# Kernel optimization log

Measured on AMD Instinct MI355X. Metric: run time of the kernel, lower is better.

## Reference

```python
import jax, jax.numpy as jnp
import numpy as np

RADII = [2, 4]
EPS = 1e-6


def _avg_pool_hw(t, k):
    # valid avg-pool with kernel k, stride 1 over the last two dims
    nd = t.ndim
    win = (1,) * (nd - 2) + (k, k)
    s = jax.lax.reduce_window(t, 0.0, jax.lax.add, win, (1,) * nd, 'VALID')
    return s / float(k * k)


def _patch_cca(x, y, r):
    B, C1, H, W = x.shape
    C2 = y.shape[1]
    k = 2 * r + 1
    pad = ((0, 0), (0, 0), (r, r), (r, r))
    xp = jnp.pad(x, pad, mode='reflect')  # (B,C1,Hp,Wp)
    yp = jnp.pad(y, pad, mode='reflect')  # (B,C2,Hp,Wp)

    # local second moments via outer products + avg pooling
    xx = _avg_pool_hw(xp[:, :, None] * xp[:, None], k)  # (B,C1,C1,H,W)
    yy = _avg_pool_hw(yp[:, :, None] * yp[:, None], k)  # (B,C2,C2,H,W)
    xy = _avg_pool_hw(xp[:, :, None] * yp[:, None], k)  # (B,C1,C2,H,W)
    xm = _avg_pool_hw(xp, k)  # (B,C1,H,W)
    ym = _avg_pool_hw(yp, k)  # (B,C2,H,W)

    cxx = xx - xm[:, :, None] * xm[:, None]
    cyy = yy - ym[:, :, None] * ym[:, None]
    cxy = xy - xm[:, :, None] * ym[:, None]

    # move matrix dims last: (B,H,W,Ci,Cj)
    cxx = jnp.transpose(cxx, (0, 3, 4, 1, 2)) + EPS * jnp.eye(C1, dtype=x.dtype)
    cyy = jnp.transpose(cyy, (0, 3, 4, 1, 2)) + EPS * jnp.eye(C2, dtype=x.dtype)
    cxy = jnp.transpose(cxy, (0, 3, 4, 1, 2))

    lx_inv = jnp.linalg.inv(jnp.linalg.cholesky(cxx))  # (B,H,W,C1,C1)
    ly_inv = jnp.linalg.inv(jnp.linalg.cholesky(cyy))  # (B,H,W,C2,C2)
    corr = jnp.einsum('bhwij,bhwjk,bhwkl->bhwil', lx_inv, cxy, ly_inv)
    diag = jnp.diagonal(corr, axis1=-2, axis2=-1)  # (B,H,W,min(C1,C2))
    sim = jnp.abs(diag).sum(-1) / min(C1, C2)  # (B,H,W)
    return sim[:, None]  # (B,1,H,W)


def setup_inputs() -> dict:
    key = jax.random.key(0)
    kx, ky = jax.random.split(key)
    B, C, H, W = 2, 6, 512, 512
    x = jax.random.normal(kx, (B, C, H, W), dtype=jnp.float32)
    y = jax.random.normal(ky, (B, C, H, W), dtype=jnp.float32)
    return {'x': x, 'y': y}


def reference(x, y):
    # stack per-radius CCA maps on a trailing axis -> (B,1,H,W,len(RADII))
    return jnp.stack([_patch_cca(x, y, r) for r in RADII], axis=-1)
```

## Files before the change

### kernel.cpp

```cpp
#include <hip/hip_runtime.h>
#include <math.h>

typedef float v2f __attribute__((ext_vector_type(2)));
typedef float v4f __attribute__((ext_vector_type(4)));

#define LT(i,j) ((i)*((i)+1)/2 + (j))

__device__ __forceinline__ int reflect512(int i) {
  int a = (i < 0) ? -i : i;
  int b = 1022 - a;
  return (a < b) ? a : b;
}

constexpr int HB   = 520;
constexpr int RSP  = HB * 4;
constexpr int PSTR = 2 * HB * HB * 4;

__global__ __launch_bounds__(256)
void prep_planar_t(const float* __restrict__ xg, const float* __restrict__ yg,
                   float* __restrict__ zb) {
  constexpr int H = 512, W = 512, HW = H * W;
  constexpr int WQ  = HB / 4;
  constexpr int PER = 2 * HB * WQ;
  const int idx = blockIdx.x * 256 + threadIdx.x;
  if (idx >= 3 * PER) return;
  const int p  = idx / PER;
  int r        = idx - p * PER;
  const int b  = r / (HB * WQ);
  r           -= b * (HB * WQ);
  const int hr = r / WQ;
  const int q  = r - hr * WQ;
  const int h  = reflect512(hr - 4);
  const int w0 = q * 4 - 4;

  float v[4][4];
  #pragma unroll
  for (int c = 0; c < 4; ++c) {
    const int ch = 4 * p + c;
    const float* src = (ch < 6 ? xg : yg)
                     + (size_t)b * 6 * HW + (size_t)(ch % 6) * HW
                     + (size_t)h * W;
    if (w0 >= 0 && w0 + 3 < W) {
      const v4f t = *(const v4f*)(src + w0);
      #pragma unroll
      for (int j = 0; j < 4; ++j) v[c][j] = t[j];
    } else {
      #pragma unroll
      for (int j = 0; j < 4; ++j) v[c][j] = src[reflect512(w0 + j)];
    }
  }

  float* o = zb + (size_t)p * PSTR + ((size_t)(b * HB + hr) * HB + q * 4) * 4;
  #pragma unroll
  for (int j = 0; j < 4; ++j) {
    v4f t = {v[0][j], v[1][j], v[2][j], v[3][j]};
    *(v4f*)(o + j * 4) = t;
  }
}

__device__ __forceinline__ float gget(const v2f* accd, const v2f* accs,
                                      int a, int b) {
  const int t = LT(a >> 1, b >> 1);
  if (((a & 1) == 0) && ((b & 1) == 0)) return accd[t].x;
  if (((a & 1) == 1) && ((b & 1) == 1)) return accd[t].y;
  if ((a & 1) == 0) return accs[t].x;
  return accs[t].y;
}

__device__ __forceinline__ void cholinv6(float* a) {
  #pragma unroll
  for (int j = 0; j < 6; ++j) {
    float d = a[LT(j,j)];
    #pragma unroll
    for (int p = 0; p < j; ++p) d -= a[LT(j,p)] * a[LT(j,p)];
    const float rd = __builtin_amdgcn_rsqf(d);
    a[LT(j,j)] = rd;
    #pragma unroll
    for (int i = j + 1; i < 6; ++i) {
      float s = a[LT(i,j)];
      #pragma unroll
      for (int p = 0; p < j; ++p) s -= a[LT(i,p)] * a[LT(j,p)];
      a[LT(i,j)] = s * rd;
    }
  }
  #pragma unroll
  for (int j = 0; j < 6; ++j) {
    #pragma unroll
    for (int i = j + 1; i < 6; ++i) {
      float s = 0.0f;
      #pragma unroll
      for (int p = j; p < i; ++p) s += a[LT(i,p)] * a[LT(p,j)];
      a[LT(i,j)] = -s * a[LT(i,i)];
    }
  }
}

template <bool ADD>
__device__ __forceinline__ void px_acc(const float* __restrict__ p,
                                       v2f* zs, v2f* accd, v2f* accs) {
  const v4f l0 = *(const v4f*)(p + 0 * PSTR);
  const v4f l1 = *(const v4f*)(p + 1 * PSTR);
  const v4f l2 = *(const v4f*)(p + 2 * PSTR);
  v2f z[6];
  z[0] = l0.lo; z[1] = l0.hi;
  z[2] = l1.lo; z[3] = l1.hi;
  z[4] = l2.lo; z[5] = l2.hi;
  #pragma unroll
  for (int q = 0; q < 6; ++q) zs[q] = ADD ? (zs[q] + z[q]) : (zs[q] - z[q]);
  int t = 0;
  #pragma unroll
  for (int Kp = 0; Kp < 6; ++Kp) {
    #pragma unroll
    for (int Pp = 0; Pp <= Kp; ++Pp) {
      const v2f c  = z[Pp];
      const v2f cs = __builtin_shufflevector(c, c, 1, 0);
      const v2f a  = ADD ? z[Kp] : -z[Kp];
      accd[t] = __builtin_elementwise_fma(a, c,  accd[t]);
      accs[t] = __builtin_elementwise_fma(a, cs, accs[t]);
      ++t;
    }
  }
}

template <int K, bool ADD>
__device__ __forceinline__ void row_acc_g(const float* __restrict__ p,
                                          v2f* zs, v2f* accd, v2f* accs) {
  #pragma unroll
  for (int dx = 0; dx < K; ++dx) px_acc<ADD>(p + dx * 4, zs, accd, accs);
}

template <int K>
__device__ __forceinline__ void extract_emit(const v2f* zs, const v2f* accd,
                                             const v2f* accs,
                                             float* ax, float* ay, float* cxy) {
  constexpr float inv_n = 1.0f / (K * K);
  float mx[6], my[6];
  #pragma unroll
  for (int i = 0; i < 6; ++i) {
    mx[i] = ((i & 1) ? zs[i >> 1].y : zs[i >> 1].x) * inv_n;
    my[i] = ((i & 1) ? zs[3 + (i >> 1)].y : zs[3 + (i >> 1)].x) * inv_n;
  }
  {
    int t = 0;
    #pragma unroll
    for (int i = 0; i < 6; ++i)
      #pragma unroll
      for (int j = 0; j <= i; ++j) {
        const float e = (i == j) ? 1e-6f : 0.0f;
        ax[t] = gget(accd, accs, i, j) * inv_n - mx[i] * mx[j] + e;
        ay[t] = gget(accd, accs, 6 + i, 6 + j) * inv_n - my[i] * my[j] + e;
        ++t;
      }
  }
  #pragma unroll
  for (int i = 0; i < 6; ++i)
    #pragma unroll
    for (int j = 0; j < 6; ++j)
      cxy[i * 6 + j] = fmaf(-mx[i], my[j], gget(accd, accs, 6 + j, i) * inv_n);
}

__device__ __forceinline__ float finish_sim(float* ax, float* ay,
                                            const float* cxy) {
  cholinv6(ax);
  cholinv6(ay);
  float sim = 0.0f;
  #pragma unroll
  for (int i = 0; i < 6; ++i) {
    float di = 0.0f;
    #pragma unroll
    for (int j = 0; j <= i; ++j) {
      float inner = 0.0f;
      #pragma unroll
      for (int k = i; k < 6; ++k) inner += cxy[j * 6 + k] * ay[LT(k, i)];
      di += ax[LT(i, j)] * inner;
    }
    sim += fabsf(di);
  }
  return sim * (1.0f / 6.0f);
}

template <int R, int V>
__device__ __forceinline__ void run(const float* __restrict__ zb,
                                    float* __restrict__ out, int b, int ri) {
  constexpr int K = 2 * R + 1;
  constexpr int H = 512, W = 512;

  const int h0 = blockIdx.y * (16 * V);
  const int w0 = blockIdx.x * 16;
  const int tx = threadIdx.x & 15;
  const int g  = threadIdx.x >> 4;
  const int hbase = h0 + g * V;
  const int wc = w0 + tx;

  const float* base = zb +
      ((size_t)(b * HB + (hbase + 4 - R)) * HB + (wc + 4 - R)) * 4;

  v2f zs[6]    = {};
  v2f accd[21] = {};
  v2f accs[21] = {};

  #pragma unroll 1
  for (int dy = 0; dy < K; ++dy)
    row_acc_g<K, true>(base + dy * RSP, zs, accd, accs);

  float ax[21], ay[21], cxy[36];
  extract_emit<K>(zs, accd, accs, ax, ay, cxy);

  #pragma unroll 1
  for (int s = 1; s < V; ++s) {
    row_acc_g<K, true >(base + (s + 2 * R) * RSP, zs, accd, accs);
    row_acc_g<K, false>(base + (s - 1)     * RSP, zs, accd, accs);
    out[((size_t)((b * H + hbase + s - 1) * W + wc)) * 2 + ri] =
        finish_sim(ax, ay, cxy);
    extract_emit<K>(zs, accd, accs, ax, ay, cxy);
  }
  out[((size_t)((b * H + hbase + V - 1) * W + wc)) * 2 + ri] =
      finish_sim(ax, ay, cxy);
}

__global__ __launch_bounds__(256, 2)
void cca_planar(const float* __restrict__ zb, float* __restrict__ out) {
  const int z = blockIdx.z;
  if (z < 2) run<2, 8>(zb, out, z, 0);
  else       run<4, 8>(zb, out, z - 2, 1);
}

extern "C" void kernel_launch(void* const* d_in, const int* in_sizes, int n_in,
                              void* d_out, int out_size, void* d_ws, size_t ws_size,
                              hipStream_t stream) {
  const float* x = (const float*)d_in[0];
  const float* y = (const float*)d_in[1];
  float* out = (float*)d_out;
  float* zb  = (float*)d_ws;

  {
    const int n = 3 * 2 * HB * (HB / 4);
    prep_planar_t<<<dim3((n + 255) / 256), dim3(256), 0, stream>>>(x, y, zb);
  }
  dim3 grid(512 / 16, 512 / (16 * 8), 4);
  cca_planar<<<grid, dim3(256), 0, stream>>>(zb, out);
}
```

Baseline: 137.4 us.

## Fuse prep and CCA kernels with a software grid barrier

Merges the planar-transpose prep kernel into the main CCA kernel. Each of the 512 blocks first does a grid-strided share of the prep work, then all blocks wait on a global atomic counter barrier before computing. This removes one kernel launch and the gap between the two kernels. In exchange it relies on all 512 blocks being co-resident, which launch_bounds(256,2) on a 256-CU part should allow. The generation counter makes the barrier reusable across calls, but it adds spin-wait and fence costs.

```diff
diff --git a/kernel.cpp b/kernel.cpp
--- a/kernel.cpp
+++ b/kernel.cpp
@@ -16,14 +16,15 @@
 constexpr int RSP  = HB * 4;
 constexpr int PSTR = 2 * HB * HB * 4;
 
-__global__ __launch_bounds__(256)
-void prep_planar_t(const float* __restrict__ xg, const float* __restrict__ yg,
-                   float* __restrict__ zb) {
+__device__ unsigned int g_bar = 0;
+
+__device__ __forceinline__ void prep_unit(int idx,
+                                          const float* __restrict__ xg,
+                                          const float* __restrict__ yg,
+                                          float* __restrict__ zb) {
   constexpr int H = 512, W = 512, HW = H * W;
   constexpr int WQ  = HB / 4;
   constexpr int PER = 2 * HB * WQ;
-  const int idx = blockIdx.x * 256 + threadIdx.x;
-  if (idx >= 3 * PER) return;
   const int p  = idx / PER;
   int r        = idx - p * PER;
   const int b  = r / (HB * WQ);
@@ -219,7 +220,29 @@
 }
 
 __global__ __launch_bounds__(256, 2)
-void cca_planar(const float* __restrict__ zb, float* __restrict__ out) {
+void cca_fused(const float* __restrict__ xg, const float* __restrict__ yg,
+               float* __restrict__ zb, float* __restrict__ out) {
+  constexpr int WQ    = HB / 4;
+  constexpr int NPREP = 3 * 2 * HB * WQ;
+  constexpr int NTHR  = 512 * 256;
+
+  const int bid = ((int)blockIdx.z * 4 + (int)blockIdx.y) * 32 + (int)blockIdx.x;
+  for (int idx = bid * 256 + (int)threadIdx.x; idx < NPREP; idx += NTHR)
+    prep_unit(idx, xg, yg, zb);
+
+  __syncthreads();
+  if (threadIdx.x == 0) {
+    __threadfence();
+    const unsigned my = __hip_atomic_fetch_add(&g_bar, 1u, __ATOMIC_ACQ_REL,
+                                               __HIP_MEMORY_SCOPE_AGENT);
+    const unsigned target = (my / 512u + 1u) * 512u;
+    while (__hip_atomic_load(&g_bar, __ATOMIC_ACQUIRE,
+                             __HIP_MEMORY_SCOPE_AGENT) < target)
+      __builtin_amdgcn_s_sleep(2);
+    __threadfence();
+  }
+  __syncthreads();
+
   const int z = blockIdx.z;
   if (z < 2) run<2, 8>(zb, out, z, 0);
   else       run<4, 8>(zb, out, z - 2, 1);
@@ -233,10 +256,6 @@
   float* out = (float*)d_out;
   float* zb  = (float*)d_ws;
 
-  {
-    const int n = 3 * 2 * HB * (HB / 4);
-    prep_planar_t<<<dim3((n + 255) / 256), dim3(256), 0, stream>>>(x, y, zb);
-  }
   dim3 grid(512 / 16, 512 / (16 * 8), 4);
-  cca_planar<<<grid, dim3(256), 0, stream>>>(zb, out);
-}
+  cca_fused<<<grid, dim3(256), 0, stream>>>(x, y, zb, out);
+}
```

After: 220.9 us. +60.8%, slower.
